# Performance work log

Hardware: AMD Instinct MI355X
Metric: run time of the kernel (lower is better)

Reference implementation:

```python
import jax, jax.numpy as jnp
import numpy as np

H = 32  # hidden size


def _gru_layer(x_seq, W_ih, W_hh, b_ih, b_hh):
    """x_seq: [B, T, in] -> outputs [B, T, H], final h [B, H]. PyTorch gate order (r, z, n)."""
    B = x_seq.shape[0]
    # Precompute input projections for all timesteps: [T, B, 3H]
    xw = jnp.einsum('bti,gi->tbg', x_seq, W_ih) + b_ih
    h0 = jnp.zeros((B, H), dtype=x_seq.dtype)

    def step(h, xw_t):
        gh = h @ W_hh.T + b_hh                       # [B, 3H]
        r = jax.nn.sigmoid(xw_t[:, :H] + gh[:, :H])
        z = jax.nn.sigmoid(xw_t[:, H:2 * H] + gh[:, H:2 * H])
        n = jnp.tanh(xw_t[:, 2 * H:] + r * gh[:, 2 * H:])
        h_new = (1.0 - z) * n + z * h
        return h_new, h_new

    h_last, ys = jax.lax.scan(step, h0, xw)
    return jnp.transpose(ys, (1, 0, 2)), h_last       # [B, T, H], [B, H]


def setup_inputs() -> dict:
    key = jax.random.key(0)
    ks = jax.random.split(key, 11)
    s = 1.0 / np.sqrt(H)  # PyTorch GRU init scale
    return {
        'x': jax.random.normal(ks[0], (4096, 512, 32), dtype=jnp.float32),
        'W_ih0': jax.random.uniform(ks[1], (96, 32), jnp.float32, -s, s),
        'W_hh0': jax.random.uniform(ks[2], (96, 32), jnp.float32, -s, s),
        'b_ih0': jax.random.uniform(ks[3], (96,), jnp.float32, -s, s),
        'b_hh0': jax.random.uniform(ks[4], (96,), jnp.float32, -s, s),
        'W_ih1': jax.random.uniform(ks[5], (96, 32), jnp.float32, -s, s),
        'W_hh1': jax.random.uniform(ks[6], (96, 32), jnp.float32, -s, s),
        'b_ih1': jax.random.uniform(ks[7], (96,), jnp.float32, -s, s),
        'b_hh1': jax.random.uniform(ks[8], (96,), jnp.float32, -s, s),
        'W_proj': jax.random.uniform(ks[9], (16, 32), jnp.float32, -s, s),
        'b_proj': jax.random.uniform(ks[10], (16,), jnp.float32, -s, s),
    }


def reference(x, W_ih0, W_hh0, b_ih0, b_hh0, W_ih1, W_hh1, b_ih1, b_hh1, W_proj, b_proj):
    y0, _ = _gru_layer(x, W_ih0, W_hh0, b_ih0, b_hh0)        # layer 0 full sequence
    _, h_last = _gru_layer(y0, W_ih1, W_hh1, b_ih1, b_hh1)   # layer 1 final hidden
    # dropout is identity in eval mode
    return h_last @ W_proj.T + b_proj                        # [B, 16]
```

## Files before the change

kernel.cpp:

```cpp
#include <hip/hip_runtime.h>

using bf16x8 = __attribute__((ext_vector_type(8))) short;
using short8 = __attribute__((ext_vector_type(8))) short;
using s16x4  = __attribute__((ext_vector_type(4))) short;
using f32x4  = __attribute__((ext_vector_type(4))) float;
using u32x4  = __attribute__((ext_vector_type(4))) unsigned;
using ull    = unsigned long long;

#define T_SEQ 512
#define MFMA(A, B, C) __builtin_amdgcn_mfma_f32_16x16x32_bf16((A), (B), (C), 0, 0, 0)

#define BARRIER()                                            \
    do {                                                     \
        __builtin_amdgcn_sched_barrier(0);                   \
        asm volatile("s_waitcnt lgkmcnt(0)" ::: "memory");   \
        __builtin_amdgcn_s_barrier();                        \
        __builtin_amdgcn_sched_barrier(0);                   \
    } while (0)

static constexpr float NL2E  = -1.44269504f;
static constexpr float N2L2E = -2.88539008f;

__device__ __forceinline__ void split8_tr(f32x4 a, f32x4 b, bf16x8& hi, bf16x8& lo) {
    u32x4 ua = __builtin_bit_cast(u32x4, a);
    u32x4 ub = __builtin_bit_cast(u32x4, b);
    u32x4 m  = {0xffff0000u, 0xffff0000u, 0xffff0000u, 0xffff0000u};
    f32x4 ra = a - __builtin_bit_cast(f32x4, ua & m);
    f32x4 rb = b - __builtin_bit_cast(f32x4, ub & m);
    short8 sa  = __builtin_bit_cast(short8, a);
    short8 sb  = __builtin_bit_cast(short8, b);
    short8 sra = __builtin_bit_cast(short8, ra);
    short8 srb = __builtin_bit_cast(short8, rb);
    hi = __builtin_shufflevector(sa, sb, 1, 3, 5, 7, 9, 11, 13, 15);
    lo = __builtin_shufflevector(sra, srb, 1, 3, 5, 7, 9, 11, 13, 15);
}

__device__ __forceinline__ void split4_tr(f32x4 a, s16x4& hi, s16x4& lo) {
    u32x4 ua = __builtin_bit_cast(u32x4, a);
    u32x4 m  = {0xffff0000u, 0xffff0000u, 0xffff0000u, 0xffff0000u};
    f32x4 ra = a - __builtin_bit_cast(f32x4, ua & m);
    short8 sa  = __builtin_bit_cast(short8, a);
    short8 sra = __builtin_bit_cast(short8, ra);
    hi = __builtin_shufflevector(sa, sa, 1, 3, 5, 7);
    lo = __builtin_shufflevector(sra, sra, 1, 3, 5, 7);
}

__device__ __forceinline__ bf16x8 combine8(ull lo8, ull hi8) {
    u32x4 v = {(unsigned)lo8, (unsigned)(lo8 >> 32),
               (unsigned)hi8, (unsigned)(hi8 >> 32)};
    return __builtin_bit_cast(bf16x8, v);
}
__device__ __forceinline__ bf16x8 combine8_sel(ull own, ull other, int m) {
    return combine8(m ? other : own, m ? own : other);
}

__device__ __forceinline__ void mfma9(const bf16x8 (&WH)[3], const bf16x8 (&WL)[3],
                                      bf16x8 inh, bf16x8 inl,
                                      f32x4 c0, f32x4 c1, f32x4 c2,
                                      f32x4& a0, f32x4& a1, f32x4& a2) {
    a0 = MFMA(WH[0], inh, c0); a1 = MFMA(WH[1], inh, c1); a2 = MFMA(WH[2], inh, c2);
    a0 = MFMA(WH[0], inl, a0); a1 = MFMA(WH[1], inl, a1); a2 = MFMA(WH[2], inl, a2);
    a0 = MFMA(WL[0], inh, a0); a1 = MFMA(WL[1], inh, a1); a2 = MFMA(WL[2], inh, a2);
}

__device__ __forceinline__ void gate4(f32x4 aR, f32x4 aZ, f32x4 iN, f32x4 sN,
                                      float (&hf)[4]) {
    float er[4], ez[4];
    #pragma unroll
    for (int j = 0; j < 4; ++j) er[j] = __builtin_amdgcn_exp2f(aR[j] * NL2E);
    #pragma unroll
    for (int j = 0; j < 4; ++j) ez[j] = __builtin_amdgcn_exp2f(aZ[j] * NL2E);
    float gr[4], gz[4];
    #pragma unroll
    for (int j = 0; j < 4; ++j) gr[j] = __builtin_amdgcn_rcpf(1.f + er[j]);
    #pragma unroll
    for (int j = 0; j < 4; ++j) gz[j] = __builtin_amdgcn_rcpf(1.f + ez[j]);
    float en[4];
    #pragma unroll
    for (int j = 0; j < 4; ++j) {
        float u = fmaf(gr[j], sN[j], iN[j]);
        en[j] = __builtin_amdgcn_exp2f(fminf(u * N2L2E, 126.f));
    }
    float qn[4];
    #pragma unroll
    for (int j = 0; j < 4; ++j) qn[j] = __builtin_amdgcn_rcpf(1.f + en[j]);
    #pragma unroll
    for (int j = 0; j < 4; ++j) {
        float nn = fmaf(en[j] * qn[j], -2.f, 1.f);
        hf[j] = fmaf(gz[j], hf[j] - nn, nn);
    }
}

__global__ __launch_bounds__(256, 1)
void gru2_quad(const float* __restrict__ x,
               const float* __restrict__ W_ih0, const float* __restrict__ W_hh0,
               const float* __restrict__ b_ih0, const float* __restrict__ b_hh0,
               const float* __restrict__ W_ih1, const float* __restrict__ W_hh1,
               const float* __restrict__ b_ih1, const float* __restrict__ b_hh1,
               const float* __restrict__ W_proj, const float* __restrict__ b_proj,
               float* __restrict__ out)
{
    const int tid  = threadIdx.x;
    const int wid  = tid >> 6;
    const int L    = wid >> 1;
    const int m    = wid & 1;
    const int lane = tid & 63;
    const int r16  = lane & 15;
    const int q    = lane >> 4;
    const int b0   = blockIdx.x * 16;

    __shared__ ull pubH_[2][2][2][64];
    __shared__ ull pubL_[2][2][2][64];

    const float* Wx = L ? W_ih1 : W_ih0;
    const float* Wh = L ? W_hh1 : W_hh0;
    const float* bx = L ? b_ih1 : b_ih0;
    const float* bh = L ? b_hh1 : b_hh0;

    bf16x8 WxH[3], WxL[3], WhH[3], WhL[3];
    f32x4 bxf[3], bhf[3];
    #pragma unroll
    for (int g = 0; g < 3; ++g) {
        const int tile = 2 * g + m;
        const float* p1 = Wx + (16 * tile + r16) * 32 + 4 * q;
        split8_tr(*(const f32x4*)p1, *(const f32x4*)(p1 + 16), WxH[g], WxL[g]);
        const float* p2 = Wh + (16 * tile + r16) * 32 + 4 * q;
        split8_tr(*(const f32x4*)p2, *(const f32x4*)(p2 + 16), WhH[g], WhL[g]);
        bxf[g] = *(const f32x4*)(bx + 16 * tile + 4 * q);
        bhf[g] = *(const f32x4*)(bh + 16 * tile + 4 * q);
    }

    #pragma unroll
    for (int g = 0; g < 3; ++g) {
        asm volatile("" : "+v"(WxH[g]), "+v"(WxL[g]));
        asm volatile("" : "+v"(WhH[g]), "+v"(WhL[g]));
        asm volatile("" : "+v"(bxf[g]), "+v"(bhf[g]));
    }

    float hf[4] = {0.f, 0.f, 0.f, 0.f};
    ull ownH = 0, ownL = 0;
    const float* xp = x + (size_t)(b0 + r16) * (T_SEQ * 32) + 4 * q;
    f32x4 xA = {}, xB = {};
    bf16x8 xh_cur = {}, xl_cur = {};

    if (L == 0) {
        f32x4 x0A = *(const f32x4*)(xp);
        f32x4 x0B = *(const f32x4*)(xp + 16);
        xA = *(const f32x4*)(xp + 32);
        xB = *(const f32x4*)(xp + 48);
        split8_tr(x0A, x0B, xh_cur, xl_cur);
        f32x4 iR, iZ, iN;
        mfma9(WxH, WxL, xh_cur, xl_cur, bxf[0], bxf[1], bxf[2], iR, iZ, iN);
        gate4(iR + bhf[0], iZ + bhf[1], iN, bhf[2], hf);
        s16x4 hi4, lo4;
        split4_tr(f32x4{hf[0], hf[1], hf[2], hf[3]}, hi4, lo4);
        ownH = __builtin_bit_cast(ull, hi4);
        ownL = __builtin_bit_cast(ull, lo4);
        pubH_[m][0][0][lane] = ownH;
        pubL_[m][0][0][lane] = ownL;
        split8_tr(xA, xB, xh_cur, xl_cur);
        xA = *(const f32x4*)(xp + 64);
        xB = *(const f32x4*)(xp + 80);
    } else {
        pubH_[m][1][1][lane] = 0;
        pubL_[m][1][1][lane] = 0;
    }

    #pragma unroll 1
    for (int t = 1; t < T_SEQ; ++t) {
        #pragma unroll
        for (int g = 0; g < 3; ++g) {
            asm volatile("" : "+v"(WxH[g]), "+v"(WxL[g]));
            asm volatile("" : "+v"(WhH[g]), "+v"(WhL[g]));
            asm volatile("" : "+v"(bxf[g]), "+v"(bhf[g]));
        }

        BARRIER();
        const int pPrev = (t - 1) & 1;
        const int pCur  = t & 1;
        f32x4 iR, iZ, iN, sR, sZ, sN;
        if (L == 0) {
            ull oH = pubH_[1 - m][0][pPrev][lane];
            ull oL = pubL_[1 - m][0][pPrev][lane];
            mfma9(WxH, WxL, xh_cur, xl_cur, bxf[0], bxf[1], bxf[2], iR, iZ, iN);
            bf16x8 Sh = combine8_sel(ownH, oH, m);
            bf16x8 Sl = combine8_sel(ownL, oL, m);
            mfma9(WhH, WhL, Sh, Sl, bhf[0], bhf[1], bhf[2], sR, sZ, sN);
            split8_tr(xA, xB, xh_cur, xl_cur);
            const int tn = (t + 2 < T_SEQ) ? t + 2 : T_SEQ - 1;
            xA = *(const f32x4*)(xp + (size_t)tn * 32);
            xB = *(const f32x4*)(xp + (size_t)tn * 32 + 16);
        } else {
            ull i0H = pubH_[0][0][pPrev][lane];
            ull i1H = pubH_[1][0][pPrev][lane];
            ull i0L = pubL_[0][0][pPrev][lane];
            ull i1L = pubL_[1][0][pPrev][lane];
            ull oH  = pubH_[1 - m][1][pCur][lane];
            ull oL  = pubL_[1 - m][1][pCur][lane];
            bf16x8 inh = combine8(i0H, i1H);
            bf16x8 inl = combine8(i0L, i1L);
            mfma9(WxH, WxL, inh, inl, bxf[0], bxf[1], bxf[2], iR, iZ, iN);
            bf16x8 Sh = combine8_sel(ownH, oH, m);
            bf16x8 Sl = combine8_sel(ownL, oL, m);
            mfma9(WhH, WhL, Sh, Sl, bhf[0], bhf[1], bhf[2], sR, sZ, sN);
        }

        gate4(sR + iR, sZ + iZ, iN, sN, hf);

        s16x4 hi4, lo4;
        split4_tr(f32x4{hf[0], hf[1], hf[2], hf[3]}, hi4, lo4);
        ownH = __builtin_bit_cast(ull, hi4);
        ownL = __builtin_bit_cast(ull, lo4);
        const int pW = (L == 0) ? pCur : pPrev;
        pubH_[m][L][pW][lane] = ownH;
        pubL_[m][L][pW][lane] = ownL;
    }

    __syncthreads();
    if (L == 1) {
        bf16x8 inh = combine8(pubH_[0][0][1][lane], pubH_[1][0][1][lane]);
        bf16x8 inl = combine8(pubL_[0][0][1][lane], pubL_[1][0][1][lane]);
        bf16x8 Sh  = combine8_sel(ownH, pubH_[1 - m][1][0][lane], m);
        bf16x8 Sl  = combine8_sel(ownL, pubL_[1 - m][1][0][lane], m);
        f32x4 iR, iZ, iN, sR, sZ, sN;
        mfma9(WxH, WxL, inh, inl, bxf[0], bxf[1], bxf[2], iR, iZ, iN);
        mfma9(WhH, WhL, Sh, Sl, bhf[0], bhf[1], bhf[2], sR, sZ, sN);
        gate4(sR + iR, sZ + iZ, iN, sN, hf);
        s16x4 hi4, lo4;
        split4_tr(f32x4{hf[0], hf[1], hf[2], hf[3]}, hi4, lo4);
        pubH_[m][1][1][lane] = __builtin_bit_cast(ull, hi4);
        pubL_[m][1][1][lane] = __builtin_bit_cast(ull, lo4);
    }
    __syncthreads();

    if (wid == 2) {
        bf16x8 Hh = combine8(pubH_[0][1][1][lane], pubH_[1][1][1][lane]);
        bf16x8 Hl = combine8(pubL_[0][1][1][lane], pubL_[1][1][1][lane]);
        const float* pp = W_proj + r16 * 32 + 4 * q;
        bf16x8 Wph, Wpl;
        split8_tr(*(const f32x4*)pp, *(const f32x4*)(pp + 16), Wph, Wpl);
        f32x4 accp = *(const f32x4*)(b_proj + 4 * q);
        accp = MFMA(Wph, Hh, accp);
        accp = MFMA(Wph, Hl, accp);
        accp = MFMA(Wpl, Hh, accp);
        #pragma unroll
        for (int rg = 0; rg < 4; ++rg)
            out[(b0 + r16) * 16 + 4 * q + rg] = accp[rg];
    }
}

extern "C" void kernel_launch(void* const* d_in, const int* in_sizes, int n_in,
                              void* d_out, int out_size, void* d_ws, size_t ws_size,
                              hipStream_t stream) {
    const float* x      = (const float*)d_in[0];
    const float* W_ih0  = (const float*)d_in[1];
    const float* W_hh0  = (const float*)d_in[2];
    const float* b_ih0  = (const float*)d_in[3];
    const float* b_hh0  = (const float*)d_in[4];
    const float* W_ih1  = (const float*)d_in[5];
    const float* W_hh1  = (const float*)d_in[6];
    const float* b_ih1  = (const float*)d_in[7];
    const float* b_hh1  = (const float*)d_in[8];
    const float* W_proj = (const float*)d_in[9];
    const float* b_proj = (const float*)d_in[10];
    float* out = (float*)d_out;

    const int nb   = in_sizes[0] / (T_SEQ * 32);
    const int grid = nb / 16;

    hipLaunchKernelGGL(gru2_quad, dim3(grid), dim3(256), 0, stream,
                       x, W_ih0, W_hh0, b_ih0, b_hh0,
                       W_ih1, W_hh1, b_ih1, b_hh1, W_proj, b_proj, out);
}
```

Measured before the change: 296.2 us.

## Split input projections into producer waves pipelined ahead of recurrent waves

Doubles the block to 8 waves. Four producer waves compute the input-side MFMA projections (x·W_ih for layer 0, y0·W_ih for layer 1) one step ahead and pass them through double-buffered LDS. Four consumer waves then run only the recurrent W_hh MFMAs and the gate math, which shortens the serial critical path per timestep. In exchange the loop runs two extra iterations, adds LDS traffic for the projections, and puts twice as many waves through every barrier.

```diff
diff --git a/kernel.cpp b/kernel.cpp
--- a/kernel.cpp
+++ b/kernel.cpp
@@ -8,6 +8,7 @@
 using ull    = unsigned long long;
 
 #define T_SEQ 512
+#define NITER 514
 #define MFMA(A, B, C) __builtin_amdgcn_mfma_f32_16x16x32_bf16((A), (B), (C), 0, 0, 0)
 
 #define BARRIER()                                            \
@@ -54,15 +55,6 @@
     return combine8(m ? other : own, m ? own : other);
 }
 
-__device__ __forceinline__ void mfma9(const bf16x8 (&WH)[3], const bf16x8 (&WL)[3],
-                                      bf16x8 inh, bf16x8 inl,
-                                      f32x4 c0, f32x4 c1, f32x4 c2,
-                                      f32x4& a0, f32x4& a1, f32x4& a2) {
-    a0 = MFMA(WH[0], inh, c0); a1 = MFMA(WH[1], inh, c1); a2 = MFMA(WH[2], inh, c2);
-    a0 = MFMA(WH[0], inl, a0); a1 = MFMA(WH[1], inl, a1); a2 = MFMA(WH[2], inl, a2);
-    a0 = MFMA(WL[0], inh, a0); a1 = MFMA(WL[1], inh, a1); a2 = MFMA(WL[2], inh, a2);
-}
-
 __device__ __forceinline__ void gate4(f32x4 aR, f32x4 aZ, f32x4 iN, f32x4 sN,
                                       float (&hf)[4]) {
     float er[4], ez[4];
@@ -91,8 +83,8 @@
     }
 }
 
-__global__ __launch_bounds__(256, 1)
-void gru2_quad(const float* __restrict__ x,
+__global__ __launch_bounds__(512, 1)
+void gru2_octo(const float* __restrict__ x,
                const float* __restrict__ W_ih0, const float* __restrict__ W_hh0,
                const float* __restrict__ b_ih0, const float* __restrict__ b_hh0,
                const float* __restrict__ W_ih1, const float* __restrict__ W_hh1,
@@ -102,7 +94,8 @@
 {
     const int tid  = threadIdx.x;
     const int wid  = tid >> 6;
-    const int L    = wid >> 1;
+    const int role = wid >> 2;
+    const int L    = (wid >> 1) & 1;
     const int m    = wid & 1;
     const int lane = tid & 63;
     const int r16  = lane & 15;
@@ -111,129 +104,141 @@
 
     __shared__ ull pubH_[2][2][2][64];
     __shared__ ull pubL_[2][2][2][64];
-
-    const float* Wx = L ? W_ih1 : W_ih0;
-    const float* Wh = L ? W_hh1 : W_hh0;
-    const float* bx = L ? b_ih1 : b_ih0;
-    const float* bh = L ? b_hh1 : b_hh0;
-
-    bf16x8 WxH[3], WxL[3], WhH[3], WhL[3];
-    f32x4 bxf[3], bhf[3];
-    #pragma unroll
-    for (int g = 0; g < 3; ++g) {
-        const int tile = 2 * g + m;
-        const float* p1 = Wx + (16 * tile + r16) * 32 + 4 * q;
-        split8_tr(*(const f32x4*)p1, *(const f32x4*)(p1 + 16), WxH[g], WxL[g]);
-        const float* p2 = Wh + (16 * tile + r16) * 32 + 4 * q;
-        split8_tr(*(const f32x4*)p2, *(const f32x4*)(p2 + 16), WhH[g], WhL[g]);
-        bxf[g] = *(const f32x4*)(bx + 16 * tile + 4 * q);
-        bhf[g] = *(const f32x4*)(bh + 16 * tile + 4 * q);
-    }
-
-    #pragma unroll
-    for (int g = 0; g < 3; ++g) {
-        asm volatile("" : "+v"(WxH[g]), "+v"(WxL[g]));
-        asm volatile("" : "+v"(WhH[g]), "+v"(WhL[g]));
-        asm volatile("" : "+v"(bxf[g]), "+v"(bhf[g]));
-    }
-
-    float hf[4] = {0.f, 0.f, 0.f, 0.f};
-    ull ownH = 0, ownL = 0;
-    const float* xp = x + (size_t)(b0 + r16) * (T_SEQ * 32) + 4 * q;
-    f32x4 xA = {}, xB = {};
-    bf16x8 xh_cur = {}, xl_cur = {};
-
-    if (L == 0) {
-        f32x4 x0A = *(const f32x4*)(xp);
-        f32x4 x0B = *(const f32x4*)(xp + 16);
-        xA = *(const f32x4*)(xp + 32);
-        xB = *(const f32x4*)(xp + 48);
-        split8_tr(x0A, x0B, xh_cur, xl_cur);
-        f32x4 iR, iZ, iN;
-        mfma9(WxH, WxL, xh_cur, xl_cur, bxf[0], bxf[1], bxf[2], iR, iZ, iN);
-        gate4(iR + bhf[0], iZ + bhf[1], iN, bhf[2], hf);
-        s16x4 hi4, lo4;
-        split4_tr(f32x4{hf[0], hf[1], hf[2], hf[3]}, hi4, lo4);
-        ownH = __builtin_bit_cast(ull, hi4);
-        ownL = __builtin_bit_cast(ull, lo4);
-        pubH_[m][0][0][lane] = ownH;
-        pubL_[m][0][0][lane] = ownL;
-        split8_tr(xA, xB, xh_cur, xl_cur);
-        xA = *(const f32x4*)(xp + 64);
-        xB = *(const f32x4*)(xp + 80);
-    } else {
-        pubH_[m][1][1][lane] = 0;
-        pubL_[m][1][1][lane] = 0;
-    }
-
-    #pragma unroll 1
-    for (int t = 1; t < T_SEQ; ++t) {
+    __shared__ f32x4 iacc[2][2][2][64][3];
+
+    if (role == 0) {
+        const float* Wh = L ? W_hh1 : W_hh0;
+        const float* bh = L ? b_hh1 : b_hh0;
+        bf16x8 WhH[3], WhL[3];
         #pragma unroll
         for (int g = 0; g < 3; ++g) {
-            asm volatile("" : "+v"(WxH[g]), "+v"(WxL[g]));
-            asm volatile("" : "+v"(WhH[g]), "+v"(WhL[g]));
-            asm volatile("" : "+v"(bxf[g]), "+v"(bhf[g]));
-        }
-
-        BARRIER();
-        const int pPrev = (t - 1) & 1;
-        const int pCur  = t & 1;
-        f32x4 iR, iZ, iN, sR, sZ, sN;
-        if (L == 0) {
-            ull oH = pubH_[1 - m][0][pPrev][lane];
-            ull oL = pubL_[1 - m][0][pPrev][lane];
-            mfma9(WxH, WxL, xh_cur, xl_cur, bxf[0], bxf[1], bxf[2], iR, iZ, iN);
+            const int tile = 2 * g + m;
+            const float* p2 = Wh + (16 * tile + r16) * 32 + 4 * q;
+            split8_tr(*(const f32x4*)p2, *(const f32x4*)(p2 + 16), WhH[g], WhL[g]);
+        }
+        f32x4 bhn = *(const f32x4*)(bh + 16 * (4 + m) + 4 * q);
+
+        pubH_[m][L][1][lane] = 0;
+        pubL_[m][L][1][lane] = 0;
+
+        float hf[4] = {0.f, 0.f, 0.f, 0.f};
+        ull ownH = 0, ownL = 0;
+        const int t0 = L ? 2 : 0;
+        const int t1 = L ? (NITER - 1) : (T_SEQ - 1);
+
+        #pragma unroll 1
+        for (int t = 0; t < NITER; ++t) {
+            BARRIER();
+            if (t < t0 || t > t1) continue;
+            const int pR = (t - 1) & 1;
+            const int pC = t & 1;
+            ull oH = pubH_[1 - m][L][pR][lane];
+            ull oL = pubL_[1 - m][L][pR][lane];
+            f32x4 cR = iacc[L][m][pC][lane][0];
+            f32x4 cZ = iacc[L][m][pC][lane][1];
+            f32x4 cN = iacc[L][m][pC][lane][2];
             bf16x8 Sh = combine8_sel(ownH, oH, m);
             bf16x8 Sl = combine8_sel(ownL, oL, m);
-            mfma9(WhH, WhL, Sh, Sl, bhf[0], bhf[1], bhf[2], sR, sZ, sN);
-            split8_tr(xA, xB, xh_cur, xl_cur);
+            f32x4 sR = MFMA(WhH[0], Sh, cR);
+            f32x4 sZ = MFMA(WhH[1], Sh, cZ);
+            f32x4 sN = MFMA(WhH[2], Sh, bhn);
+            sR = MFMA(WhH[0], Sl, sR); sZ = MFMA(WhH[1], Sl, sZ); sN = MFMA(WhH[2], Sl, sN);
+            sR = MFMA(WhL[0], Sh, sR); sZ = MFMA(WhL[1], Sh, sZ); sN = MFMA(WhL[2], Sh, sN);
+            gate4(sR, sZ, cN, sN, hf);
+            s16x4 hi4, lo4;
+            split4_tr(f32x4{hf[0], hf[1], hf[2], hf[3]}, hi4, lo4);
+            ownH = __builtin_bit_cast(ull, hi4);
+            ownL = __builtin_bit_cast(ull, lo4);
+            pubH_[m][L][pC][lane] = ownH;
+            pubL_[m][L][pC][lane] = ownL;
+        }
+    } else if (L == 0) {
+        bf16x8 WxH[3], WxL[3];
+        f32x4 cRb, cZb, cNb;
+        #pragma unroll
+        for (int g = 0; g < 3; ++g) {
+            const int tile = 2 * g + m;
+            const float* p1 = W_ih0 + (16 * tile + r16) * 32 + 4 * q;
+            split8_tr(*(const f32x4*)p1, *(const f32x4*)(p1 + 16), WxH[g], WxL[g]);
+        }
+        cRb = *(const f32x4*)(b_ih0 + 16 * m + 4 * q)
+            + *(const f32x4*)(b_hh0 + 16 * m + 4 * q);
+        cZb = *(const f32x4*)(b_ih0 + 16 * (2 + m) + 4 * q)
+            + *(const f32x4*)(b_hh0 + 16 * (2 + m) + 4 * q);
+        cNb = *(const f32x4*)(b_ih0 + 16 * (4 + m) + 4 * q);
+
+        const float* xp = x + (size_t)(b0 + r16) * (T_SEQ * 32) + 4 * q;
+        {
+            f32x4 xA0 = *(const f32x4*)(xp);
+            f32x4 xB0 = *(const f32x4*)(xp + 16);
+            bf16x8 xh, xl;
+            split8_tr(xA0, xB0, xh, xl);
+            f32x4 iR = MFMA(WxH[0], xh, cRb);
+            f32x4 iZ = MFMA(WxH[1], xh, cZb);
+            f32x4 iN = MFMA(WxH[2], xh, cNb);
+            iR = MFMA(WxH[0], xl, iR); iZ = MFMA(WxH[1], xl, iZ); iN = MFMA(WxH[2], xl, iN);
+            iR = MFMA(WxL[0], xh, iR); iZ = MFMA(WxL[1], xh, iZ); iN = MFMA(WxL[2], xh, iN);
+            iacc[0][m][0][lane][0] = iR;
+            iacc[0][m][0][lane][1] = iZ;
+            iacc[0][m][0][lane][2] = iN;
+        }
+        f32x4 xA = *(const f32x4*)(xp + 32);
+        f32x4 xB = *(const f32x4*)(xp + 48);
+
+        #pragma unroll 1
+        for (int t = 0; t < NITER; ++t) {
+            BARRIER();
+            if (t > T_SEQ - 2) continue;
+            bf16x8 xh, xl;
+            split8_tr(xA, xB, xh, xl);
             const int tn = (t + 2 < T_SEQ) ? t + 2 : T_SEQ - 1;
             xA = *(const f32x4*)(xp + (size_t)tn * 32);
             xB = *(const f32x4*)(xp + (size_t)tn * 32 + 16);
-        } else {
-            ull i0H = pubH_[0][0][pPrev][lane];
-            ull i1H = pubH_[1][0][pPrev][lane];
-            ull i0L = pubL_[0][0][pPrev][lane];
-            ull i1L = pubL_[1][0][pPrev][lane];
-            ull oH  = pubH_[1 - m][1][pCur][lane];
-            ull oL  = pubL_[1 - m][1][pCur][lane];
-            bf16x8 inh = combine8(i0H, i1H);
-            bf16x8 inl = combine8(i0L, i1L);
-            mfma9(WxH, WxL, inh, inl, bxf[0], bxf[1], bxf[2], iR, iZ, iN);
-            bf16x8 Sh = combine8_sel(ownH, oH, m);
-            bf16x8 Sl = combine8_sel(ownL, oL, m);
-            mfma9(WhH, WhL, Sh, Sl, bhf[0], bhf[1], bhf[2], sR, sZ, sN);
-        }
-
-        gate4(sR + iR, sZ + iZ, iN, sN, hf);
-
-        s16x4 hi4, lo4;
-        split4_tr(f32x4{hf[0], hf[1], hf[2], hf[3]}, hi4, lo4);
-        ownH = __builtin_bit_cast(ull, hi4);
-        ownL = __builtin_bit_cast(ull, lo4);
-        const int pW = (L == 0) ? pCur : pPrev;
-        pubH_[m][L][pW][lane] = ownH;
-        pubL_[m][L][pW][lane] = ownL;
+            f32x4 iR = MFMA(WxH[0], xh, cRb);
+            f32x4 iZ = MFMA(WxH[1], xh, cZb);
+            f32x4 iN = MFMA(WxH[2], xh, cNb);
+            iR = MFMA(WxH[0], xl, iR); iZ = MFMA(WxH[1], xl, iZ); iN = MFMA(WxH[2], xl, iN);
+            iR = MFMA(WxL[0], xh, iR); iZ = MFMA(WxL[1], xh, iZ); iN = MFMA(WxL[2], xh, iN);
+            const int wp = (t + 1) & 1;
+            iacc[0][m][wp][lane][0] = iR;
+            iacc[0][m][wp][lane][1] = iZ;
+            iacc[0][m][wp][lane][2] = iN;
+        }
+    } else {
+        bf16x8 WxH[3], WxL[3];
+        f32x4 cRb, cZb, cNb;
+        #pragma unroll
+        for (int g = 0; g < 3; ++g) {
+            const int tile = 2 * g + m;
+            const float* p1 = W_ih1 + (16 * tile + r16) * 32 + 4 * q;
+            split8_tr(*(const f32x4*)p1, *(const f32x4*)(p1 + 16), WxH[g], WxL[g]);
+        }
+        cRb = *(const f32x4*)(b_ih1 + 16 * m + 4 * q)
+            + *(const f32x4*)(b_hh1 + 16 * m + 4 * q);
+        cZb = *(const f32x4*)(b_ih1 + 16 * (2 + m) + 4 * q)
+            + *(const f32x4*)(b_hh1 + 16 * (2 + m) + 4 * q);
+        cNb = *(const f32x4*)(b_ih1 + 16 * (4 + m) + 4 * q);
+
+        #pragma unroll 1
+        for (int t = 0; t < NITER; ++t) {
+            BARRIER();
+            if (t < 1 || t > T_SEQ) continue;
+            const int p = (t - 1) & 1;
+            bf16x8 inh = combine8(pubH_[0][0][p][lane], pubH_[1][0][p][lane]);
+            bf16x8 inl = combine8(pubL_[0][0][p][lane], pubL_[1][0][p][lane]);
+            f32x4 iR = MFMA(WxH[0], inh, cRb);
+            f32x4 iZ = MFMA(WxH[1], inh, cZb);
+            f32x4 iN = MFMA(WxH[2], inh, cNb);
+            iR = MFMA(WxH[0], inl, iR); iZ = MFMA(WxH[1], inl, iZ); iN = MFMA(WxH[2], inl, iN);
+            iR = MFMA(WxL[0], inh, iR); iZ = MFMA(WxL[1], inh, iZ); iN = MFMA(WxL[2], inh, iN);
+            iacc[1][m][p][lane][0] = iR;
+            iacc[1][m][p][lane][1] = iZ;
+            iacc[1][m][p][lane][2] = iN;
+        }
     }
 
     __syncthreads();
-    if (L == 1) {
-        bf16x8 inh = combine8(pubH_[0][0][1][lane], pubH_[1][0][1][lane]);
-        bf16x8 inl = combine8(pubL_[0][0][1][lane], pubL_[1][0][1][lane]);
-        bf16x8 Sh  = combine8_sel(ownH, pubH_[1 - m][1][0][lane], m);
-        bf16x8 Sl  = combine8_sel(ownL, pubL_[1 - m][1][0][lane], m);
-        f32x4 iR, iZ, iN, sR, sZ, sN;
-        mfma9(WxH, WxL, inh, inl, bxf[0], bxf[1], bxf[2], iR, iZ, iN);
-        mfma9(WhH, WhL, Sh, Sl, bhf[0], bhf[1], bhf[2], sR, sZ, sN);
-        gate4(sR + iR, sZ + iZ, iN, sN, hf);
-        s16x4 hi4, lo4;
-        split4_tr(f32x4{hf[0], hf[1], hf[2], hf[3]}, hi4, lo4);
-        pubH_[m][1][1][lane] = __builtin_bit_cast(ull, hi4);
-        pubL_[m][1][1][lane] = __builtin_bit_cast(ull, lo4);
-    }
-    __syncthreads();
-
-    if (wid == 2) {
+    if (wid == 0) {
         bf16x8 Hh = combine8(pubH_[0][1][1][lane], pubH_[1][1][1][lane]);
         bf16x8 Hl = combine8(pubL_[0][1][1][lane], pubL_[1][1][1][lane]);
         const float* pp = W_proj + r16 * 32 + 4 * q;
@@ -268,7 +273,7 @@
     const int nb   = in_sizes[0] / (T_SEQ * 32);
     const int grid = nb / 16;
 
-    hipLaunchKernelGGL(gru2_quad, dim3(grid), dim3(256), 0, stream,
+    hipLaunchKernelGGL(gru2_octo, dim3(grid), dim3(512), 0, stream,
                        x, W_ih0, W_hh0, b_ih0, b_hh0,
                        W_ih1, W_hh1, b_ih1, b_hh1, W_proj, b_proj, out);
 }
```

Result: faster. 282.2 us (-4.8%).
